# Performance work log

Measured on AMD Instinct MI355X. Metric: run time of the kernel, lower is better.

## Reference

```python
import jax, jax.numpy as jnp
import numpy as np

B, CW_DIM = 256, 8192
DIM_EMBED = 128
DICT_SIZE = 4096
DIM_CODES = CW_DIM // DIM_EMBED  # 64


def setup_inputs() -> dict:
    key = jax.random.key(0)
    k1, k2 = jax.random.split(key)
    x = jax.random.normal(k1, (B, CW_DIM), dtype=jnp.float32)
    dictionary = jax.random.normal(k2, (DIM_CODES, DICT_SIZE, DIM_EMBED), dtype=jnp.float32)
    return {"x": x, "dictionary": dictionary}


def reference(x, dictionary):
    """VQVAE.quantise (eval mode): pairwise sq-distance -> argmin -> gather + one-hot.

    x: [B, cw_dim], dictionary: [C, S, E] with cw_dim = C*E.
    Returns (cw_embed [B, C*E], one_hot_idx [B, C, S]).
    """
    Bb, D = x.shape
    C, S, E = dictionary.shape
    xr = x.reshape(Bb, C, E)                                   # [B, C, E]
    x_sq = jnp.sum(xr * xr, axis=-1, keepdims=True)            # [B, C, 1]
    d_sq = jnp.sum(dictionary * dictionary, axis=-1)           # [C, S]
    cross = jnp.einsum('bce,cse->bcs', xr, dictionary)         # [B, C, S] (GEMM)
    dist = x_sq + d_sq[None, :, :] - 2.0 * cross               # [B, C, S]
    idx = jnp.argmin(dist, axis=-1)                            # [B, C]
    # gather nearest codes: dictionary[c, idx[b,c]] -> [B, C, E]
    code_ids = jnp.arange(C)[None, :]                          # [1, C]
    cw_embed = dictionary[code_ids, idx]                       # [B, C, E]
    cw_embed = cw_embed.reshape(Bb, C * E)                     # [B, cw_dim]
    one_hot_idx = jax.nn.one_hot(idx, S, dtype=x.dtype)        # [B, C, S]
    return cw_embed, one_hot_idx
```

## Files before the change

### kernel.cpp

```cpp
#include <hip/hip_runtime.h>
#include <stdint.h>


#define B_SZ 256
#define C_SZ 64
#define E_SZ 128
#define S_SZ 4096
#define CW   8192
#define TS   64
#define LDB  136

typedef __attribute__((ext_vector_type(4))) float    float4a;
typedef __attribute__((ext_vector_type(8))) _Float16 half8;

__device__ __forceinline__ void split8(float4a f0, float4a f1, half8& hi, half8& lo) {
    #pragma unroll
    for (int j = 0; j < 4; ++j) {
        _Float16 h0 = (_Float16)f0[j];
        hi[j]     = h0;
        lo[j]     = (_Float16)(f0[j] - (float)h0);
        _Float16 h1 = (_Float16)f1[j];
        hi[4 + j] = h1;
        lo[4 + j] = (_Float16)(f1[j] - (float)h1);
    }
}

__global__ __launch_bounds__(512, 4) void argmin_mfma(
    const float* __restrict__ x,
    const float* __restrict__ dict,
    float* __restrict__ cw_out,
    float* __restrict__ oh)
{
    __shared__ __attribute__((aligned(16))) _Float16 bh[2][TS * LDB];
    __shared__ __attribute__((aligned(16))) _Float16 bl[2][TS * LDB];
    __shared__ float dsqp[2][TS][8];
    float* rv = reinterpret_cast<float*>(bh);
    int*   ri = reinterpret_cast<int*>(bl);

    const int tid   = threadIdx.x;
    const int lane  = tid & 63;
    const int quad  = lane >> 4;
    const int l15   = lane & 15;
    const int wid   = tid >> 6;
    const int mhalf = wid & 1;
    const int nquad = wid >> 1;
    const int c     = blockIdx.x & 63;
    const int btile = (blockIdx.x >> 6) & 3;
    const int shalf = blockIdx.x >> 8;
    const int sbase = shalf * 2048;

    int m_attr[4], n_attr[4];
    {
        half8 ones, enc;
        #pragma unroll
        for (int j = 0; j < 8; ++j) { ones[j] = (_Float16)1.0f; enc[j] = (_Float16)(float)l15; }
        float4a z = {0.f, 0.f, 0.f, 0.f};
        float4a pr = __builtin_amdgcn_mfma_f32_16x16x32_f16(enc, ones, z, 0, 0, 0);
        float4a pc = __builtin_amdgcn_mfma_f32_16x16x32_f16(ones, enc, z, 0, 0, 0);
        #pragma unroll
        for (int r = 0; r < 4; ++r) {
            m_attr[r] = (int)(pr[r] * 0.03125f + 0.5f);
            n_attr[r] = (int)(pc[r] * 0.03125f + 0.5f);
        }
    }

    half8 ah[2][4], al[2][4];
    #pragma unroll
    for (int mi = 0; mi < 2; ++mi) {
        int b = btile * 64 + mhalf * 32 + mi * 16 + l15;
        const float* xr = x + (size_t)b * CW + c * E_SZ;
        #pragma unroll
        for (int kk = 0; kk < 4; ++kk) {
            float4a f0 = *reinterpret_cast<const float4a*>(xr + kk * 32 + quad * 8);
            float4a f1 = *reinterpret_cast<const float4a*>(xr + kk * 32 + quad * 8 + 4);
            split8(f0, f1, ah[mi][kk], al[mi][kk]);
        }
    }

    const int srow = tid >> 3;
    const int kq   = (tid & 7) * 16;
    const float* drow = dict + ((size_t)c * S_SZ + sbase + srow) * E_SZ + kq;

    float* ohb = oh + ((size_t)(btile * 64) * C_SZ + c) * S_SZ + sbase;
    const size_t oh_bstride = (size_t)C_SZ * S_SZ;

    float4a pf[4];
    #pragma unroll
    for (int ck = 0; ck < 4; ++ck)
        pf[ck] = *reinterpret_cast<const float4a*>(drow + ck * 4);
    {
        float dp = 0.f;
        #pragma unroll
        for (int ck = 0; ck < 2; ++ck) {
            half8 h, l;
            split8(pf[2 * ck], pf[2 * ck + 1], h, l);
            #pragma unroll
            for (int j = 0; j < 4; ++j) {
                dp = fmaf(pf[2 * ck][j], pf[2 * ck][j], dp);
                dp = fmaf(pf[2 * ck + 1][j], pf[2 * ck + 1][j], dp);
            }
            *reinterpret_cast<half8*>(&bh[0][srow * LDB + kq + ck * 8]) = h;
            *reinterpret_cast<half8*>(&bl[0][srow * LDB + kq + ck * 8]) = l;
        }
        dsqp[0][srow][tid & 7] = dp;
    }

    float bestv[8];
    int   besti[8];
    #pragma unroll
    for (int i = 0; i < 8; ++i) { bestv[i] = 3.4e38f; besti[i] = 0; }

    __syncthreads();

    int cur = 0;
    for (int it = 0; it < 32; ++it) {
        if (it + 1 < 32) {
            const float* dr = drow + (size_t)(it + 1) * (TS * E_SZ);
            #pragma unroll
            for (int ck = 0; ck < 4; ++ck)
                pf[ck] = *reinterpret_cast<const float4a*>(dr + ck * 4);
        }

        {
            float4a zz = {0.f, 0.f, 0.f, 0.f};
            float* z0 = ohb + (size_t)(it * 2) * oh_bstride;
            float* z1 = z0 + oh_bstride;
            __builtin_nontemporal_store(zz, reinterpret_cast<float4a*>(z0) + tid);
            __builtin_nontemporal_store(zz, reinterpret_cast<float4a*>(z1) + tid);
        }

        const _Float16* bhc = bh[cur];
        const _Float16* blc = bl[cur];
        float4a acc[2] = {{0.f,0.f,0.f,0.f},{0.f,0.f,0.f,0.f}};
        __builtin_amdgcn_s_setprio(1);
        #pragma unroll
        for (int kk = 0; kk < 4; ++kk) {
            const int sl = nquad * 16 + l15;
            half8 bhf = *reinterpret_cast<const half8*>(bhc + sl * LDB + kk * 32 + quad * 8);
            half8 blf = *reinterpret_cast<const half8*>(blc + sl * LDB + kk * 32 + quad * 8);
            #pragma unroll
            for (int mi = 0; mi < 2; ++mi) {
                acc[mi] = __builtin_amdgcn_mfma_f32_16x16x32_f16(
                    ah[mi][kk], bhf, acc[mi], 0, 0, 0);
                acc[mi] = __builtin_amdgcn_mfma_f32_16x16x32_f16(
                    ah[mi][kk], blf, acc[mi], 0, 0, 0);
                acc[mi] = __builtin_amdgcn_mfma_f32_16x16x32_f16(
                    al[mi][kk], bhf, acc[mi], 0, 0, 0);
            }
        }
        __builtin_amdgcn_s_setprio(0);

        #pragma unroll
        for (int r = 0; r < 4; ++r) {
            const int sl = nquad * 16 + n_attr[r];
            float4a qa = *reinterpret_cast<const float4a*>(&dsqp[cur][sl][0]);
            float4a qb = *reinterpret_cast<const float4a*>(&dsqp[cur][sl][4]);
            float dsq = ((qa[0] + qa[1]) + (qa[2] + qa[3]))
                      + ((qb[0] + qb[1]) + (qb[2] + qb[3]));
            int sg = sbase + it * TS + sl;
            #pragma unroll
            for (int mi = 0; mi < 2; ++mi) {
                float dist = dsq - 2.0f * acc[mi][r];
                int slot = mi * 4 + r;
                if (dist < bestv[slot]) { bestv[slot] = dist; besti[slot] = sg; }
            }
        }

        if (it + 1 < 32) {
            const int nb = cur ^ 1;
            float dp = 0.f;
            #pragma unroll
            for (int ck = 0; ck < 2; ++ck) {
                half8 h, l;
                split8(pf[2 * ck], pf[2 * ck + 1], h, l);
                #pragma unroll
                for (int j = 0; j < 4; ++j) {
                    dp = fmaf(pf[2 * ck][j], pf[2 * ck][j], dp);
                    dp = fmaf(pf[2 * ck + 1][j], pf[2 * ck + 1][j], dp);
                }
                *reinterpret_cast<half8*>(&bh[nb][srow * LDB + kq + ck * 8]) = h;
                *reinterpret_cast<half8*>(&bl[nb][srow * LDB + kq + ck * 8]) = l;
            }
            dsqp[nb][srow][tid & 7] = dp;
        }
        __syncthreads();
        cur ^= 1;
    }


    #pragma unroll
    for (int mi = 0; mi < 2; ++mi)
        #pragma unroll
        for (int r = 0; r < 4; ++r) {
            int row = mhalf * 32 + mi * 16 + m_attr[r];
            int col = nquad * 16 + n_attr[r];
            rv[row * 64 + col] = bestv[mi * 4 + r];
            ri[row * 64 + col] = besti[mi * 4 + r];
        }
    __syncthreads();

    if (tid < 64) {
        float bv = 3.4e38f; int bi = 0x7fffffff;
        for (int j = 0; j < 64; ++j) {
            float v = rv[tid * 64 + j];
            int   i = ri[tid * 64 + j];
            if (v < bv || (v == bv && i < bi)) { bv = v; bi = i; }
        }
        float* cp = cw_out + (size_t)(btile * 64 + tid) * CW + c * E_SZ + shalf * 2;
        cp[0] = bv;
        cp[1] = __int_as_float(bi);
    }
}

__global__ __launch_bounds__(256) void finalize(
    const float* __restrict__ dict,
    float* __restrict__ cw_out,
    float* __restrict__ oh)
{
    __shared__ int fid[64];
    const int c     = blockIdx.x & 63;
    const int btile = blockIdx.x >> 6;
    const int tid   = threadIdx.x;

    if (tid < 64) {
        const float* cp = cw_out + (size_t)(btile * 64 + tid) * CW + c * E_SZ;
        float d0 = cp[0]; int i0 = __float_as_int(cp[1]);
        float d1 = cp[2]; int i1 = __float_as_int(cp[3]);
        int bi = (d1 < d0) ? i1 : i0;
        fid[tid] = bi;
        oh[((size_t)(btile * 64 + tid) * C_SZ + c) * S_SZ + bi] = 1.0f;
    }
    __syncthreads();

    const int row = tid >> 2, q = tid & 3;
    const int bi = fid[row];
    const float4a* src = reinterpret_cast<const float4a*>(
        dict + ((size_t)c * S_SZ + bi) * E_SZ) + q * 8;
    float4a* dst = reinterpret_cast<float4a*>(
        cw_out + (size_t)(btile * 64 + row) * CW + c * E_SZ) + q * 8;
    #pragma unroll
    for (int j = 0; j < 8; ++j) dst[j] = src[j];
}

extern "C" void kernel_launch(void* const* d_in, const int* in_sizes, int n_in,
                              void* d_out, int out_size, void* d_ws, size_t ws_size,
                              hipStream_t stream) {
    const float* x    = (const float*)d_in[0];
    const float* dict = (const float*)d_in[1];
    float* out = (float*)d_out;
    float* oh  = out + (size_t)B_SZ * CW;

    argmin_mfma<<<dim3(512), dim3(512), 0, stream>>>(x, dict, out, oh);
    finalize<<<dim3(256), dim3(256), 0, stream>>>(dict, out, oh);
}
```

Baseline: 500.3 us.

## Cover all 256 batch rows per block and XOR-swizzle dictionary LDS tiles

Each block now handles every batch row for one codebook and a quarter of the dictionary entries, instead of 64 rows and half the entries. Each dictionary tile is therefore loaded and split to fp16 once for the whole batch rather than four times, and the grid shrinks to 256 blocks. The LDS padding is replaced by an XOR swizzle to avoid bank conflicts, and the finalize step merges four partial argmins instead of two. In exchange, per-thread register pressure roughly doubles (16 accumulators plus A fragments), occupancy drops to 2 blocks per CU, and 256 blocks may underfill the GPU.

```diff
diff --git a/kernel.cpp b/kernel.cpp
--- a/kernel.cpp
+++ b/kernel.cpp
@@ -8,10 +8,15 @@
 #define S_SZ 4096
 #define CW   8192
 #define TS   64
-#define LDB  136
+#define SPB  1024
+#define LDB  128
 
 typedef __attribute__((ext_vector_type(4))) float    float4a;
 typedef __attribute__((ext_vector_type(8))) _Float16 half8;
+
+__device__ __forceinline__ int swz(int row, int cf16) {
+    return row * LDB + (cf16 ^ ((row & 7) << 3));
+}
 
 __device__ __forceinline__ void split8(float4a f0, float4a f1, half8& hi, half8& lo) {
     #pragma unroll
@@ -25,7 +30,7 @@
     }
 }
 
-__global__ __launch_bounds__(512, 4) void argmin_mfma(
+__global__ __launch_bounds__(512, 2) void argmin_mfma(
     const float* __restrict__ x,
     const float* __restrict__ dict,
     float* __restrict__ cw_out,
@@ -33,7 +38,7 @@
 {
     __shared__ __attribute__((aligned(16))) _Float16 bh[2][TS * LDB];
     __shared__ __attribute__((aligned(16))) _Float16 bl[2][TS * LDB];
-    __shared__ float dsqp[2][TS][8];
+    __shared__ __attribute__((aligned(16))) float dsqp[2][TS][8];
     float* rv = reinterpret_cast<float*>(bh);
     int*   ri = reinterpret_cast<int*>(bl);
 
@@ -42,12 +47,11 @@
     const int quad  = lane >> 4;
     const int l15   = lane & 15;
     const int wid   = tid >> 6;
-    const int mhalf = wid & 1;
-    const int nquad = wid >> 1;
+    const int mq    = wid & 3;
+    const int nh    = wid >> 2;
     const int c     = blockIdx.x & 63;
-    const int btile = (blockIdx.x >> 6) & 3;
-    const int shalf = blockIdx.x >> 8;
-    const int sbase = shalf * 2048;
+    const int squad = blockIdx.x >> 6;
+    const int sbase = squad * SPB;
 
     int m_attr[4], n_attr[4];
     {
@@ -64,10 +68,10 @@
         }
     }
 
-    half8 ah[2][4], al[2][4];
-    #pragma unroll
-    for (int mi = 0; mi < 2; ++mi) {
-        int b = btile * 64 + mhalf * 32 + mi * 16 + l15;
+    half8 ah[4][4], al[4][4];
+    #pragma unroll
+    for (int mi = 0; mi < 4; ++mi) {
+        int b = mq * 64 + mi * 16 + l15;
         const float* xr = x + (size_t)b * CW + c * E_SZ;
         #pragma unroll
         for (int kk = 0; kk < 4; ++kk) {
@@ -79,10 +83,8 @@
 
     const int srow = tid >> 3;
     const int kq   = (tid & 7) * 16;
+    const int q8   = tid & 7;
     const float* drow = dict + ((size_t)c * S_SZ + sbase + srow) * E_SZ + kq;
-
-    float* ohb = oh + ((size_t)(btile * 64) * C_SZ + c) * S_SZ + sbase;
-    const size_t oh_bstride = (size_t)C_SZ * S_SZ;
 
     float4a pf[4];
     #pragma unroll
@@ -99,22 +101,22 @@
                 dp = fmaf(pf[2 * ck][j], pf[2 * ck][j], dp);
                 dp = fmaf(pf[2 * ck + 1][j], pf[2 * ck + 1][j], dp);
             }
-            *reinterpret_cast<half8*>(&bh[0][srow * LDB + kq + ck * 8]) = h;
-            *reinterpret_cast<half8*>(&bl[0][srow * LDB + kq + ck * 8]) = l;
-        }
-        dsqp[0][srow][tid & 7] = dp;
-    }
-
-    float bestv[8];
-    int   besti[8];
-    #pragma unroll
-    for (int i = 0; i < 8; ++i) { bestv[i] = 3.4e38f; besti[i] = 0; }
+            *reinterpret_cast<half8*>(&bh[0][swz(srow, kq + ck * 8)]) = h;
+            *reinterpret_cast<half8*>(&bl[0][swz(srow, kq + ck * 8)]) = l;
+        }
+        dsqp[0][srow][q8] = dp;
+    }
+
+    float bestv[16];
+    int   besti[16];
+    #pragma unroll
+    for (int i = 0; i < 16; ++i) { bestv[i] = 3.4e38f; besti[i] = 0; }
 
     __syncthreads();
 
     int cur = 0;
-    for (int it = 0; it < 32; ++it) {
-        if (it + 1 < 32) {
+    for (int it = 0; it < 16; ++it) {
+        if (it + 1 < 16) {
             const float* dr = drow + (size_t)(it + 1) * (TS * E_SZ);
             #pragma unroll
             for (int ck = 0; ck < 4; ++ck)
@@ -122,51 +124,64 @@
         }
 
         {
+            const int zrow = it * 16 + (tid >> 5);
+            const int t5   = tid & 31;
+            float* zb = oh + ((size_t)zrow * C_SZ + c) * S_SZ + sbase;
             float4a zz = {0.f, 0.f, 0.f, 0.f};
-            float* z0 = ohb + (size_t)(it * 2) * oh_bstride;
-            float* z1 = z0 + oh_bstride;
-            __builtin_nontemporal_store(zz, reinterpret_cast<float4a*>(z0) + tid);
-            __builtin_nontemporal_store(zz, reinterpret_cast<float4a*>(z1) + tid);
+            #pragma unroll
+            for (int j = 0; j < 8; ++j)
+                __builtin_nontemporal_store(zz, reinterpret_cast<float4a*>(zb) + t5 + j * 32);
         }
 
         const _Float16* bhc = bh[cur];
         const _Float16* blc = bl[cur];
-        float4a acc[2] = {{0.f,0.f,0.f,0.f},{0.f,0.f,0.f,0.f}};
+        float4a acc[4][2] = {{{0.f,0.f,0.f,0.f},{0.f,0.f,0.f,0.f}},
+                             {{0.f,0.f,0.f,0.f},{0.f,0.f,0.f,0.f}},
+                             {{0.f,0.f,0.f,0.f},{0.f,0.f,0.f,0.f}},
+                             {{0.f,0.f,0.f,0.f},{0.f,0.f,0.f,0.f}}};
         __builtin_amdgcn_s_setprio(1);
         #pragma unroll
         for (int kk = 0; kk < 4; ++kk) {
-            const int sl = nquad * 16 + l15;
-            half8 bhf = *reinterpret_cast<const half8*>(bhc + sl * LDB + kk * 32 + quad * 8);
-            half8 blf = *reinterpret_cast<const half8*>(blc + sl * LDB + kk * 32 + quad * 8);
-            #pragma unroll
-            for (int mi = 0; mi < 2; ++mi) {
-                acc[mi] = __builtin_amdgcn_mfma_f32_16x16x32_f16(
-                    ah[mi][kk], bhf, acc[mi], 0, 0, 0);
-                acc[mi] = __builtin_amdgcn_mfma_f32_16x16x32_f16(
-                    ah[mi][kk], blf, acc[mi], 0, 0, 0);
-                acc[mi] = __builtin_amdgcn_mfma_f32_16x16x32_f16(
-                    al[mi][kk], bhf, acc[mi], 0, 0, 0);
-            }
+            half8 bhf[2], blf[2];
+            #pragma unroll
+            for (int ni = 0; ni < 2; ++ni) {
+                const int sl = nh * 32 + ni * 16 + l15;
+                bhf[ni] = *reinterpret_cast<const half8*>(bhc + swz(sl, kk * 32 + quad * 8));
+                blf[ni] = *reinterpret_cast<const half8*>(blc + swz(sl, kk * 32 + quad * 8));
+            }
+            #pragma unroll
+            for (int mi = 0; mi < 4; ++mi)
+                #pragma unroll
+                for (int ni = 0; ni < 2; ++ni) {
+                    acc[mi][ni] = __builtin_amdgcn_mfma_f32_16x16x32_f16(
+                        ah[mi][kk], bhf[ni], acc[mi][ni], 0, 0, 0);
+                    acc[mi][ni] = __builtin_amdgcn_mfma_f32_16x16x32_f16(
+                        ah[mi][kk], blf[ni], acc[mi][ni], 0, 0, 0);
+                    acc[mi][ni] = __builtin_amdgcn_mfma_f32_16x16x32_f16(
+                        al[mi][kk], bhf[ni], acc[mi][ni], 0, 0, 0);
+                }
         }
         __builtin_amdgcn_s_setprio(0);
 
         #pragma unroll
-        for (int r = 0; r < 4; ++r) {
-            const int sl = nquad * 16 + n_attr[r];
-            float4a qa = *reinterpret_cast<const float4a*>(&dsqp[cur][sl][0]);
-            float4a qb = *reinterpret_cast<const float4a*>(&dsqp[cur][sl][4]);
-            float dsq = ((qa[0] + qa[1]) + (qa[2] + qa[3]))
-                      + ((qb[0] + qb[1]) + (qb[2] + qb[3]));
-            int sg = sbase + it * TS + sl;
-            #pragma unroll
-            for (int mi = 0; mi < 2; ++mi) {
-                float dist = dsq - 2.0f * acc[mi][r];
-                int slot = mi * 4 + r;
-                if (dist < bestv[slot]) { bestv[slot] = dist; besti[slot] = sg; }
-            }
-        }
-
-        if (it + 1 < 32) {
+        for (int ni = 0; ni < 2; ++ni)
+            #pragma unroll
+            for (int r = 0; r < 4; ++r) {
+                const int sl = nh * 32 + ni * 16 + n_attr[r];
+                float4a qa = *reinterpret_cast<const float4a*>(&dsqp[cur][sl][0]);
+                float4a qb = *reinterpret_cast<const float4a*>(&dsqp[cur][sl][4]);
+                float dsq = ((qa[0] + qa[1]) + (qa[2] + qa[3]))
+                          + ((qb[0] + qb[1]) + (qb[2] + qb[3]));
+                int sg = sbase + it * TS + sl;
+                #pragma unroll
+                for (int mi = 0; mi < 4; ++mi) {
+                    float dist = dsq - 2.0f * acc[mi][ni][r];
+                    int slot = mi * 4 + r;
+                    if (dist < bestv[slot]) { bestv[slot] = dist; besti[slot] = sg; }
+                }
+            }
+
+        if (it + 1 < 16) {
             const int nb = cur ^ 1;
             float dp = 0.f;
             #pragma unroll
@@ -178,10 +193,10 @@
                     dp = fmaf(pf[2 * ck][j], pf[2 * ck][j], dp);
                     dp = fmaf(pf[2 * ck + 1][j], pf[2 * ck + 1][j], dp);
                 }
-                *reinterpret_cast<half8*>(&bh[nb][srow * LDB + kq + ck * 8]) = h;
-                *reinterpret_cast<half8*>(&bl[nb][srow * LDB + kq + ck * 8]) = l;
-            }
-            dsqp[nb][srow][tid & 7] = dp;
+                *reinterpret_cast<half8*>(&bh[nb][swz(srow, kq + ck * 8)]) = h;
+                *reinterpret_cast<half8*>(&bl[nb][swz(srow, kq + ck * 8)]) = l;
+            }
+            dsqp[nb][srow][q8] = dp;
         }
         __syncthreads();
         cur ^= 1;
@@ -189,24 +204,25 @@
 
 
     #pragma unroll
-    for (int mi = 0; mi < 2; ++mi)
+    for (int mi = 0; mi < 4; ++mi)
         #pragma unroll
         for (int r = 0; r < 4; ++r) {
-            int row = mhalf * 32 + mi * 16 + m_attr[r];
-            int col = nquad * 16 + n_attr[r];
-            rv[row * 64 + col] = bestv[mi * 4 + r];
-            ri[row * 64 + col] = besti[mi * 4 + r];
+            int row = mq * 64 + mi * 16 + m_attr[r];
+            int col = nh * 16 + n_attr[r];
+            rv[col * 256 + row] = bestv[mi * 4 + r];
+            ri[col * 256 + row] = besti[mi * 4 + r];
         }
     __syncthreads();
 
-    if (tid < 64) {
+    if (tid < 256) {
         float bv = 3.4e38f; int bi = 0x7fffffff;
-        for (int j = 0; j < 64; ++j) {
-            float v = rv[tid * 64 + j];
-            int   i = ri[tid * 64 + j];
+        #pragma unroll 4
+        for (int j = 0; j < 32; ++j) {
+            float v = rv[j * 256 + tid];
+            int   i = ri[j * 256 + tid];
             if (v < bv || (v == bv && i < bi)) { bv = v; bi = i; }
         }
-        float* cp = cw_out + (size_t)(btile * 64 + tid) * CW + c * E_SZ + shalf * 2;
+        float* cp = cw_out + (size_t)tid * CW + c * E_SZ + squad * 2;
         cp[0] = bv;
         cp[1] = __int_as_float(bi);
     }
@@ -223,12 +239,16 @@
     const int tid   = threadIdx.x;
 
     if (tid < 64) {
-        const float* cp = cw_out + (size_t)(btile * 64 + tid) * CW + c * E_SZ;
-        float d0 = cp[0]; int i0 = __float_as_int(cp[1]);
-        float d1 = cp[2]; int i1 = __float_as_int(cp[3]);
-        int bi = (d1 < d0) ? i1 : i0;
+        const int row = btile * 64 + tid;
+        const float* cp = cw_out + (size_t)row * CW + c * E_SZ;
+        float bv = cp[0]; int bi = __float_as_int(cp[1]);
+        #pragma unroll
+        for (int k = 1; k < 4; ++k) {
+            float v = cp[2 * k];
+            if (v < bv) { bv = v; bi = __float_as_int(cp[2 * k + 1]); }
+        }
         fid[tid] = bi;
-        oh[((size_t)(btile * 64 + tid) * C_SZ + c) * S_SZ + bi] = 1.0f;
+        oh[((size_t)row * C_SZ + c) * S_SZ + bi] = 1.0f;
     }
     __syncthreads();
 
@@ -250,6 +270,6 @@
     float* out = (float*)d_out;
     float* oh  = out + (size_t)B_SZ * CW;
 
-    argmin_mfma<<<dim3(512), dim3(512), 0, stream>>>(x, dict, out, oh);
+    argmin_mfma<<<dim3(256), dim3(512), 0, stream>>>(x, dict, out, oh);
     finalize<<<dim3(256), dim3(256), 0, stream>>>(dict, out, oh);
 }
```

Result: faster. 437.3 us (-12.6%).
